# Performance work log

Measured on AMD Instinct MI355X. Metric: run time of the kernel, lower is better.

Reference implementation:

```python
import jax, jax.numpy as jnp
import numpy as np

N = 100000      # nodes
E = 1600000     # edges (before self-loops)
IN_DIM = 128
HID = 32
HEADS = 4
OUT_DIM = 64
NEG_SLOPE = 0.2  # PyG GATConv default


def setup_inputs() -> dict:
    key = jax.random.key(0)
    ks = jax.random.split(key, 12)
    s1 = 1.0 / np.sqrt(IN_DIM).astype(np.float32)
    s2 = 1.0 / np.sqrt(HEADS * HID).astype(np.float32)
    return {
        "x": jax.random.normal(ks[0], (N, IN_DIM), jnp.float32),
        "edge_index": jax.random.randint(ks[1], (2, E), 0, N, dtype=jnp.int64),
        "W1": jax.random.normal(ks[2], (IN_DIM, HEADS * HID), jnp.float32) * s1,
        "att_src1": jax.random.normal(ks[3], (HEADS, HID), jnp.float32) * 0.1,
        "att_dst1": jax.random.normal(ks[4], (HEADS, HID), jnp.float32) * 0.1,
        "b1": jnp.zeros((HEADS * HID,), jnp.float32),
        "W2": jax.random.normal(ks[5], (HEADS * HID, OUT_DIM), jnp.float32) * s2,
        "att_src2": jax.random.normal(ks[6], (1, OUT_DIM), jnp.float32) * 0.1,
        "att_dst2": jax.random.normal(ks[7], (1, OUT_DIM), jnp.float32) * 0.1,
        "b2": jnp.zeros((OUT_DIM,), jnp.float32),
    }


def _gat_layer(x, src, dst, W, att_src, att_dst, bias, heads, out_ch, concat):
    # x: [N, F_in] -> h: [N, H, C]
    n = x.shape[0]
    h = (x @ W).reshape(n, heads, out_ch)
    # per-node attention logits, [N, H]
    a_src = jnp.einsum("nhc,hc->nh", h, att_src)
    a_dst = jnp.einsum("nhc,hc->nh", h, att_dst)
    # edge logits + LeakyReLU, [E, H]
    e = a_src[src] + a_dst[dst]
    e = jnp.where(e >= 0, e, NEG_SLOPE * e)
    # segment softmax over incoming edges of each dst node
    m = jax.ops.segment_max(e, dst, num_segments=n)          # [N, H]
    e = jnp.exp(e - m[dst])
    denom = jax.ops.segment_sum(e, dst, num_segments=n)      # [N, H]
    alpha = e / (denom[dst] + 1e-16)                          # [E, H]
    # weighted scatter-aggregate of source messages -> [N, H, C]
    out = jax.ops.segment_sum(h[src] * alpha[:, :, None], dst, num_segments=n)
    if concat:
        out = out.reshape(n, heads * out_ch)
    else:
        out = out.mean(axis=1)
    return out + bias


def reference(x, edge_index, W1, att_src1, att_dst1, b1, W2, att_src2, att_dst2, b2):
    n = x.shape[0]
    # PyG GATConv adds self-loops by default
    loops = jnp.arange(n, dtype=edge_index.dtype)
    src = jnp.concatenate([edge_index[0], loops])
    dst = jnp.concatenate([edge_index[1], loops])
    h = _gat_layer(x, src, dst, W1, att_src1, att_dst1, b1, HEADS, HID, concat=True)
    h = jax.nn.elu(h)
    # dropout p=0.5 is identity in eval mode (training=False)
    out = _gat_layer(h, src, dst, W2, att_src2, att_dst2, b2, 1, OUT_DIM, concat=False)
    return out
```

## Files before the change

kernel.cpp:

```cpp
#include <hip/hip_runtime.h>
#include <hip/hip_bf16.h>
#include <hip/hip_fp16.h>

#define NEG 0.2f
#define L2E 1.44269504f
#define BSH 9
#define BNODES 512
#define MAXC 16384
#define CHUNK 4096

typedef __attribute__((ext_vector_type(8))) _Float16 half8v;
typedef __attribute__((ext_vector_type(4))) short short4v;
typedef __attribute__((ext_vector_type(4))) float f32x4;

__device__ __forceinline__ float leaky(float e) { return fmaxf(e, NEG * e); }
__device__ __forceinline__ ushort f2h(float f) {
    __half h = __float2half(f);
    return *reinterpret_cast<ushort*>(&h);
}
__device__ __forceinline__ float edgep(float l, float adv, float e0) {
    return __builtin_amdgcn_exp2f(leaky(l + adv) - e0);
}

__device__ __forceinline__ void fma8(float* acc, float a, uint4 h) {
    unsigned wv[4] = { h.x, h.y, h.z, h.w };
    #pragma unroll
    for (int j = 0; j < 4; j++) {
        __half2 hh = *reinterpret_cast<__half2*>(&wv[j]);
        float lo = __half2float(__low2half(hh));
        float hi = __half2float(__high2half(hh));
        acc[2 * j]     = fmaf(a, lo, acc[2 * j]);
        acc[2 * j + 1] = fmaf(a, hi, acc[2 * j + 1]);
    }
}


__global__ void k_zerob(int* __restrict__ bcnt) {
    bcnt[threadIdx.x] = 0;
}

__global__ __launch_bounds__(256) void k_bucket(const int* __restrict__ src, const int* __restrict__ dst,
                                                int E, unsigned int* __restrict__ bbuf,
                                                int* __restrict__ bcnt) {
    __shared__ int hcnt[256], hoff[256], gbase[256], sh[256];
    __shared__ unsigned int lbuf[CHUNK];
    __shared__ unsigned char map[CHUNK];
    int tid = threadIdx.x;
    hcnt[tid] = 0;
    __syncthreads();
    int e0 = blockIdx.x * CHUNK;
    unsigned int pk[16];
    int sl[16];
    unsigned char bb[16];
    #pragma unroll
    for (int r = 0; r < 16; r++) {
        int i = e0 + r * 256 + tid;
        sl[r] = -1; pk[r] = 0; bb[r] = 0;
        if (i < E) {
            int s = src[i], d = dst[i];
            int b = d >> BSH;
            pk[r] = ((unsigned int)(d & (BNODES - 1)) << 17) | (unsigned int)s;
            bb[r] = (unsigned char)b;
            sl[r] = atomicAdd(&hcnt[b], 1);
        }
    }
    __syncthreads();
    int v = hcnt[tid];
    sh[tid] = v;
    __syncthreads();
    for (int off = 1; off < 256; off <<= 1) {
        int t = (tid >= off) ? sh[tid - off] : 0;
        __syncthreads();
        sh[tid] += t;
        __syncthreads();
    }
    hoff[tid] = sh[tid] - v;
    if (v > 0) gbase[tid] = atomicAdd(&bcnt[tid], v);
    __syncthreads();
    #pragma unroll
    for (int r = 0; r < 16; r++) {
        if (sl[r] >= 0) {
            int pos = hoff[bb[r]] + sl[r];
            lbuf[pos] = pk[r];
            map[pos] = bb[r];
        }
    }
    int total = sh[255];
    __syncthreads();
    for (int j = tid; j < total; j += 256) {
        int lo = map[j];
        int p = gbase[lo] + (j - hoff[lo]);
        if (p < MAXC) bbuf[(size_t)lo * MAXC + p] = lbuf[j];
    }
}

__global__ __launch_bounds__(256) void k_hist(const unsigned int* __restrict__ bbuf,
                                              const int* __restrict__ bcnt, int n,
                                              int* __restrict__ deg) {
    __shared__ int hist[BNODES];
    int b = blockIdx.x, tid = threadIdx.x;
    hist[tid] = 0; hist[tid + 256] = 0;
    __syncthreads();
    int cnt = min(bcnt[b], MAXC);
    const unsigned int* p = bbuf + (size_t)b * MAXC;
    for (int i = tid; i < cnt; i += 256) atomicAdd(&hist[p[i] >> 17], 1);
    __syncthreads();
    int n0 = b << BSH;
    if (n0 + tid < n) deg[n0 + tid] = hist[tid];
    if (n0 + 256 + tid < n) deg[n0 + 256 + tid] = hist[tid + 256];
}

__global__ void k_scan1(const int* __restrict__ deg, int n, int* __restrict__ rs, int* __restrict__ bsum) {
    __shared__ int sh[256];
    int tid = threadIdx.x;
    int base = blockIdx.x * 1024 + tid * 4;
    int v0 = (base + 0 < n) ? deg[base + 0] : 0;
    int v1 = (base + 1 < n) ? deg[base + 1] : 0;
    int v2 = (base + 2 < n) ? deg[base + 2] : 0;
    int v3 = (base + 3 < n) ? deg[base + 3] : 0;
    int s = v0 + v1 + v2 + v3;
    sh[tid] = s;
    __syncthreads();
    for (int off = 1; off < 256; off <<= 1) {
        int t = (tid >= off) ? sh[tid - off] : 0;
        __syncthreads();
        sh[tid] += t;
        __syncthreads();
    }
    int ex = sh[tid] - s;
    if (base + 0 < n) rs[base + 0] = ex;
    if (base + 1 < n) rs[base + 1] = ex + v0;
    if (base + 2 < n) rs[base + 2] = ex + v0 + v1;
    if (base + 3 < n) rs[base + 3] = ex + v0 + v1 + v2;
    if (tid == 255) bsum[blockIdx.x] = sh[255];
}

__global__ void k_scan2(int* __restrict__ bsum, int nb) {
    __shared__ int sh[256];
    int tid = threadIdx.x;
    int v = (tid < nb) ? bsum[tid] : 0;
    sh[tid] = v;
    __syncthreads();
    for (int off = 1; off < 256; off <<= 1) {
        int t = (tid >= off) ? sh[tid - off] : 0;
        __syncthreads();
        sh[tid] += t;
        __syncthreads();
    }
    if (tid < nb) bsum[tid] = sh[tid] - v;
}

__global__ void k_scan3(int* __restrict__ rs, const int* __restrict__ bsum, int n, int E) {
    int i = blockIdx.x * blockDim.x + threadIdx.x;
    if (i < n) rs[i] += bsum[i >> 10];
    if (i == n) rs[n] = E;
}

__global__ __launch_bounds__(256) void k_csr(const unsigned int* __restrict__ bbuf,
                                             const int* __restrict__ bcnt, const int* __restrict__ rs,
                                             int n, int* __restrict__ csr) {
    __shared__ int off[BNODES], cur[BNODES];
    __shared__ unsigned int obuf[MAXC];
    int b = blockIdx.x, tid = threadIdx.x;
    int n0 = b << BSH;
    int segbase = rs[n0];
    off[tid]       = rs[min(n0 + tid, n)] - segbase;
    off[tid + 256] = rs[min(n0 + 256 + tid, n)] - segbase;
    cur[tid] = 0; cur[tid + 256] = 0;
    __syncthreads();
    int cnt = min(bcnt[b], MAXC);
    const unsigned int* p = bbuf + (size_t)b * MAXC;
    for (int i = tid; i < cnt; i += 256) {
        unsigned int e = p[i];
        int l = e >> 17;
        int s = atomicAdd(&cur[l], 1);
        obuf[off[l] + s] = e & 0x1FFFFu;
    }
    __syncthreads();
    for (int i = tid; i < cnt; i += 256) csr[segbase + i] = (int)obuf[i];
}

__global__ __launch_bounds__(256) void k_gemm1(const float* __restrict__ x, const float* __restrict__ W,
                                               const float* __restrict__ attS, const float* __restrict__ attD,
                                               ushort* __restrict__ h1b, float* __restrict__ as1,
                                               float* __restrict__ ad1, int n) {
    __shared__ ushort Wt[128 * 136];
    int tid = threadIdx.x;
    #pragma unroll 4
    for (int it = 0; it < 64; it++) {
        int idx = tid + 256 * it;
        int k = idx >> 7, nn = idx & 127;
        Wt[nn * 136 + k] = f2h(W[idx]);
    }
    __syncthreads();
    int lane = tid & 63;
    int wid = tid >> 6;
    int l15 = lane & 15, g = lane >> 4;
    int R0 = blockIdx.x * 128 + wid * 32;
    f32x4 acc[2][8];
    #pragma unroll
    for (int f = 0; f < 2; f++)
        #pragma unroll
        for (int nf = 0; nf < 8; nf++) acc[f][nf] = (f32x4){0.f, 0.f, 0.f, 0.f};
    size_t mclamp[2];
    mclamp[0] = (size_t)((R0 + l15 < n) ? R0 + l15 : n - 1);
    mclamp[1] = (size_t)((R0 + 16 + l15 < n) ? R0 + 16 + l15 : n - 1);
    #pragma unroll
    for (int ks = 0; ks < 4; ks++) {
        half8v xb[2];
        #pragma unroll
        for (int f = 0; f < 2; f++) {
            const float4* xp = (const float4*)(x + mclamp[f] * 128 + ks * 32 + g * 8);
            float4 a0 = xp[0], a1 = xp[1];
            half8v v;
            v[0] = (_Float16)a0.x; v[1] = (_Float16)a0.y; v[2] = (_Float16)a0.z; v[3] = (_Float16)a0.w;
            v[4] = (_Float16)a1.x; v[5] = (_Float16)a1.y; v[6] = (_Float16)a1.z; v[7] = (_Float16)a1.w;
            xb[f] = v;
        }
        #pragma unroll
        for (int nf = 0; nf < 8; nf++) {
            half8v wv = *(const half8v*)(&Wt[(16 * nf + l15) * 136 + ks * 32 + g * 8]);
            acc[0][nf] = __builtin_amdgcn_mfma_f32_16x16x32_f16(wv, xb[0], acc[0][nf], 0, 0, 0);
            acc[1][nf] = __builtin_amdgcn_mfma_f32_16x16x32_f16(wv, xb[1], acc[1][nf], 0, 0, 0);
        }
    }
    #pragma unroll
    for (int f = 0; f < 2; f++) {
        int m = R0 + 16 * f + l15;
        bool ok = m < n;
        float pS[4] = {0.f, 0.f, 0.f, 0.f}, pD[4] = {0.f, 0.f, 0.f, 0.f};
        #pragma unroll
        for (int nf = 0; nf < 8; nf++) {
            int n0 = 16 * nf + 4 * g;
            f32x4 a = acc[f][nf];
            if (ok) {
                short4v s4;
                s4[0] = (short)f2h(a[0]); s4[1] = (short)f2h(a[1]);
                s4[2] = (short)f2h(a[2]); s4[3] = (short)f2h(a[3]);
                *(short4v*)(h1b + (size_t)m * 128 + n0) = s4;
            }
            float4 vS = *(const float4*)(attS + n0);
            float4 vD = *(const float4*)(attD + n0);
            int hd = nf >> 1;
            pS[hd] += a[0] * vS.x + a[1] * vS.y + a[2] * vS.z + a[3] * vS.w;
            pD[hd] += a[0] * vD.x + a[1] * vD.y + a[2] * vD.z + a[3] * vD.w;
        }
        #pragma unroll
        for (int h = 0; h < 4; h++) {
            pS[h] += __shfl_xor(pS[h], 16, 64); pS[h] += __shfl_xor(pS[h], 32, 64);
            pD[h] += __shfl_xor(pD[h], 16, 64); pD[h] += __shfl_xor(pD[h], 32, 64);
        }
        if (ok && g == 0) {
            *(float4*)(as1 + (size_t)m * 4) = make_float4(pS[0] * L2E, pS[1] * L2E, pS[2] * L2E, pS[3] * L2E);
            *(float4*)(ad1 + (size_t)m * 4) = make_float4(pD[0] * L2E, pD[1] * L2E, pD[2] * L2E, pD[3] * L2E);
        }
    }
}

__global__ __launch_bounds__(256) void k_agg1(const int* __restrict__ rs, const int* __restrict__ csr,
                                              const ushort* __restrict__ h1b,
                                              const float* __restrict__ as1, const float* __restrict__ ad1,
                                              const float* __restrict__ b1,
                                              ushort* __restrict__ o1b, int n) {
    int w = (blockIdx.x * 256 + threadIdx.x) >> 6;
    w = __builtin_amdgcn_readfirstlane(w);
    if (w >= n) return;
    int lane = threadIdx.x & 63;
    int g = lane >> 4, q = lane & 15;
    int hd = q >> 2;
    unsigned qoff = 8u * (unsigned)q;
    float adv = ad1[(unsigned)(w * 4 + hd)];
    float e0 = leaky(as1[(unsigned)(w * 4 + hd)] + adv);
    float acc0[8], acc1[8];
    float den0 = 0.f, den1 = 0.f;
    #pragma unroll
    for (int c = 0; c < 8; c++) { acc0[c] = 0.f; acc1[c] = 0.f; }
    if (g == 0) {
        uint4 hv = *(const uint4*)(h1b + (((unsigned)w << 7) + qoff));
        fma8(acc0, 1.0f, hv);
        den0 = 1.0f;
    }
    int beg = rs[w], end = rs[w + 1];
    int i = beg;
    for (; i + 8 <= end; i += 8) {
        int ea = i + g, eb = i + 4 + g;
        int sa = csr[ea], sb = csr[eb];
        float pa = edgep(as1[(unsigned)(sa * 4 + hd)], adv, e0);
        float pb = edgep(as1[(unsigned)(sb * 4 + hd)], adv, e0);
        uint4 ha = *(const uint4*)(h1b + (((unsigned)sa << 7) + qoff));
        uint4 hb = *(const uint4*)(h1b + (((unsigned)sb << 7) + qoff));
        fma8(acc0, pa, ha);
        fma8(acc1, pb, hb);
        den0 += pa; den1 += pb;
    }
    if (i < end) {
        int ea = i + g;
        int ea2 = min(ea, end - 1);
        int sa = csr[ea2];
        float pa = (ea < end) ? edgep(as1[(unsigned)(sa * 4 + hd)], adv, e0) : 0.f;
        uint4 ha = *(const uint4*)(h1b + (((unsigned)sa << 7) + qoff));
        fma8(acc0, pa, ha);
        den0 += pa;
        if (i + 4 < end) {
            int eb = i + 4 + g;
            int eb2 = min(eb, end - 1);
            int sb = csr[eb2];
            float pb = (eb < end) ? edgep(as1[(unsigned)(sb * 4 + hd)], adv, e0) : 0.f;
            uint4 hb = *(const uint4*)(h1b + (((unsigned)sb << 7) + qoff));
            fma8(acc1, pb, hb);
            den1 += pb;
        }
    }
    float den = den0 + den1;
    den += __shfl_xor(den, 16, 64);
    den += __shfl_xor(den, 32, 64);
    #pragma unroll
    for (int c = 0; c < 8; c++) {
        float v = acc0[c] + acc1[c];
        v += __shfl_xor(v, 16, 64);
        v += __shfl_xor(v, 32, 64);
        acc0[c] = v;
    }
    if (g == 0) {
        float inv = 1.0f / den;
        float4 bv0 = *(const float4*)(b1 + 8 * q);
        float4 bv1 = *(const float4*)(b1 + 8 * q + 4);
        float o[8] = { acc0[0] * inv + bv0.x, acc0[1] * inv + bv0.y,
                       acc0[2] * inv + bv0.z, acc0[3] * inv + bv0.w,
                       acc0[4] * inv + bv1.x, acc0[5] * inv + bv1.y,
                       acc0[6] * inv + bv1.z, acc0[7] * inv + bv1.w };
        ushort st[8];
        #pragma unroll
        for (int c = 0; c < 8; c++) {
            float e = (o[c] > 0.f) ? o[c] : (__expf(o[c]) - 1.f);
            st[c] = f2h(e);
        }
        *(uint4*)(o1b + (((unsigned)w << 7) + qoff)) = *(uint4*)st;
    }
}

__global__ __launch_bounds__(256) void k_gemm2(const ushort* __restrict__ o1b, const float* __restrict__ W,
                                               const float* __restrict__ attS, const float* __restrict__ attD,
                                               ushort* __restrict__ h2b, float* __restrict__ as2,
                                               float* __restrict__ ad2, int n) {
    __shared__ ushort Wt[64 * 136];
    int tid = threadIdx.x;
    #pragma unroll 4
    for (int it = 0; it < 32; it++) {
        int idx = tid + 256 * it;
        int k = idx >> 6, nn = idx & 63;
        Wt[nn * 136 + k] = f2h(W[idx]);
    }
    __syncthreads();
    int lane = tid & 63;
    int wid = tid >> 6;
    int l15 = lane & 15, g = lane >> 4;
    int R0 = blockIdx.x * 128 + wid * 32;
    f32x4 acc[2][4];
    #pragma unroll
    for (int f = 0; f < 2; f++)
        #pragma unroll
        for (int nf = 0; nf < 4; nf++) acc[f][nf] = (f32x4){0.f, 0.f, 0.f, 0.f};
    size_t mclamp[2];
    mclamp[0] = (size_t)((R0 + l15 < n) ? R0 + l15 : n - 1);
    mclamp[1] = (size_t)((R0 + 16 + l15 < n) ? R0 + 16 + l15 : n - 1);
    #pragma unroll
    for (int ks = 0; ks < 4; ks++) {
        half8v xb[2];
        xb[0] = *(const half8v*)(o1b + mclamp[0] * 128 + ks * 32 + g * 8);
        xb[1] = *(const half8v*)(o1b + mclamp[1] * 128 + ks * 32 + g * 8);
        #pragma unroll
        for (int nf = 0; nf < 4; nf++) {
            half8v wv = *(const half8v*)(&Wt[(16 * nf + l15) * 136 + ks * 32 + g * 8]);
            acc[0][nf] = __builtin_amdgcn_mfma_f32_16x16x32_f16(wv, xb[0], acc[0][nf], 0, 0, 0);
            acc[1][nf] = __builtin_amdgcn_mfma_f32_16x16x32_f16(wv, xb[1], acc[1][nf], 0, 0, 0);
        }
    }
    #pragma unroll
    for (int f = 0; f < 2; f++) {
        int m = R0 + 16 * f + l15;
        bool ok = m < n;
        float pS = 0.f, pD = 0.f;
        #pragma unroll
        for (int nf = 0; nf < 4; nf++) {
            int n0 = 16 * nf + 4 * g;
            f32x4 a = acc[f][nf];
            if (ok) {
                short4v s4;
                s4[0] = (short)f2h(a[0]); s4[1] = (short)f2h(a[1]);
                s4[2] = (short)f2h(a[2]); s4[3] = (short)f2h(a[3]);
                *(short4v*)(h2b + (size_t)m * 64 + n0) = s4;
            }
            float4 vS = *(const float4*)(attS + n0);
            float4 vD = *(const float4*)(attD + n0);
            pS += a[0] * vS.x + a[1] * vS.y + a[2] * vS.z + a[3] * vS.w;
            pD += a[0] * vD.x + a[1] * vD.y + a[2] * vD.z + a[3] * vD.w;
        }
        pS += __shfl_xor(pS, 16, 64); pS += __shfl_xor(pS, 32, 64);
        pD += __shfl_xor(pD, 16, 64); pD += __shfl_xor(pD, 32, 64);
        if (ok && g == 0) {
            as2[m] = pS * L2E;
            ad2[m] = pD * L2E;
        }
    }
}

__global__ __launch_bounds__(256) void k_agg2(const int* __restrict__ rs, const int* __restrict__ csr,
                                              const ushort* __restrict__ h2b,
                                              const float* __restrict__ as2, const float* __restrict__ ad2,
                                              const float* __restrict__ b2,
                                              float* __restrict__ out, int n) {
    int w = (blockIdx.x * 256 + threadIdx.x) >> 6;
    w = __builtin_amdgcn_readfirstlane(w);
    if (w >= n) return;
    int lane = threadIdx.x & 63;
    int g = lane >> 3, q = lane & 7;
    unsigned qoff = 8u * (unsigned)q;
    float adv = ad2[w];
    float e0 = leaky(as2[w] + adv);
    float acc0[8], acc1[8];
    float den0 = 0.f, den1 = 0.f;
    #pragma unroll
    for (int c = 0; c < 8; c++) { acc0[c] = 0.f; acc1[c] = 0.f; }
    if (g == 0) {
        uint4 hv = *(const uint4*)(h2b + (((unsigned)w << 6) + qoff));
        fma8(acc0, 1.0f, hv);
        den0 = 1.0f;
    }
    int beg = rs[w], end = rs[w + 1];
    int i = beg;
    for (; i + 16 <= end; i += 16) {
        int ea = i + g, eb = i + 8 + g;
        int sa = csr[ea], sb = csr[eb];
        float pa = edgep(as2[(unsigned)sa], adv, e0);
        float pb = edgep(as2[(unsigned)sb], adv, e0);
        uint4 ha = *(const uint4*)(h2b + (((unsigned)sa << 6) + qoff));
        uint4 hb = *(const uint4*)(h2b + (((unsigned)sb << 6) + qoff));
        fma8(acc0, pa, ha);
        fma8(acc1, pb, hb);
        den0 += pa; den1 += pb;
    }
    for (; i < end; i += 8) {
        int e = i + g;
        int e2 = min(e, end - 1);
        int s = csr[e2];
        float p = (e < end) ? edgep(as2[(unsigned)s], adv, e0) : 0.f;
        uint4 hv = *(const uint4*)(h2b + (((unsigned)s << 6) + qoff));
        fma8(acc0, p, hv);
        den0 += p;
    }
    float den = den0 + den1;
    den += __shfl_xor(den, 8, 64);
    den += __shfl_xor(den, 16, 64);
    den += __shfl_xor(den, 32, 64);
    #pragma unroll
    for (int c = 0; c < 8; c++) {
        float v = acc0[c] + acc1[c];
        v += __shfl_xor(v, 8, 64);
        v += __shfl_xor(v, 16, 64);
        v += __shfl_xor(v, 32, 64);
        acc0[c] = v;
    }
    if (g == 0) {
        float inv = 1.0f / den;
        float4 bv0 = *(const float4*)(b2 + 8 * q);
        float4 bv1 = *(const float4*)(b2 + 8 * q + 4);
        float4 o0 = make_float4(acc0[0] * inv + bv0.x, acc0[1] * inv + bv0.y,
                                acc0[2] * inv + bv0.z, acc0[3] * inv + bv0.w);
        float4 o1 = make_float4(acc0[4] * inv + bv1.x, acc0[5] * inv + bv1.y,
                                acc0[6] * inv + bv1.z, acc0[7] * inv + bv1.w);
        *(float4*)(out + (size_t)w * 64 + 8 * q) = o0;
        *(float4*)(out + (size_t)w * 64 + 8 * q + 4) = o1;
    }
}

extern "C" void kernel_launch(void* const* d_in, const int* in_sizes, int n_in,
                              void* d_out, int out_size, void* d_ws, size_t ws_size,
                              hipStream_t stream) {
    const float* x     = (const float*)d_in[0];
    const int*   ei    = (const int*)d_in[1];
    const float* W1    = (const float*)d_in[2];
    const float* attS1 = (const float*)d_in[3];
    const float* attD1 = (const float*)d_in[4];
    const float* b1    = (const float*)d_in[5];
    const float* W2    = (const float*)d_in[6];
    const float* attS2 = (const float*)d_in[7];
    const float* attD2 = (const float*)d_in[8];
    const float* b2    = (const float*)d_in[9];
    float* out = (float*)d_out;

    int n = in_sizes[0] / 128;
    int E = in_sizes[1] / 2;
    const int* srcp = ei;
    const int* dstp = ei + E;
    int nbuck = (n + BNODES - 1) >> BSH;

    char* ws = (char*)d_ws;
    size_t off = 0;
    auto A = [&](size_t bytes) -> void* {
        void* p = ws + off;
        off = (off + bytes + 255) & ~(size_t)255;
        return p;
    };
    int* rs      = (int*)A((size_t)(n + 1) * 4);
    int* deg     = (int*)A((size_t)n * 4);
    int* bcnt    = (int*)A(1024);
    int* bsum    = (int*)A(1024);
    int* csr     = (int*)A((size_t)E * 4);
    float* as1   = (float*)A((size_t)n * 16);
    float* ad1   = (float*)A((size_t)n * 16);
    float* as2   = (float*)A((size_t)n * 4);
    float* ad2   = (float*)A((size_t)n * 4);
    unsigned int* bbuf = (unsigned int*)A((size_t)nbuck * MAXC * 4);
    ushort* h1b  = (ushort*)A((size_t)n * 128 * 2);
    ushort* o1b  = (ushort*)A((size_t)n * 128 * 2);
    ushort* h2b  = h1b;

    int nb = (n + 1023) / 1024;

    hipLaunchKernelGGL(k_zerob, dim3(1), dim3(256), 0, stream, bcnt);
    hipLaunchKernelGGL(k_bucket, dim3((E + CHUNK - 1) / CHUNK), dim3(256), 0, stream, srcp, dstp, E, bbuf, bcnt);
    hipLaunchKernelGGL(k_hist, dim3(nbuck), dim3(256), 0, stream, bbuf, bcnt, n, deg);
    hipLaunchKernelGGL(k_scan1, dim3(nb), dim3(256), 0, stream, deg, n, rs, bsum);
    hipLaunchKernelGGL(k_scan2, dim3(1), dim3(256), 0, stream, bsum, nb);
    hipLaunchKernelGGL(k_scan3, dim3((n + 1 + 255) / 256), dim3(256), 0, stream, rs, bsum, n, E);
    hipLaunchKernelGGL(k_csr, dim3(nbuck), dim3(256), 0, stream, bbuf, bcnt, rs, n, csr);

    hipLaunchKernelGGL(k_gemm1, dim3((n + 127) / 128), dim3(256), 0, stream, x, W1, attS1, attD1, h1b, as1, ad1, n);
    hipLaunchKernelGGL(k_agg1, dim3((n * 64 + 255) / 256), dim3(256), 0, stream, rs, csr, h1b, as1, ad1, b1, o1b, n);
    hipLaunchKernelGGL(k_gemm2, dim3((n + 127) / 128), dim3(256), 0, stream, o1b, W2, attS2, attD2, h2b, as2, ad2, n);
    hipLaunchKernelGGL(k_agg2, dim3((n * 64 + 255) / 256), dim3(256), 0, stream, rs, csr, h2b, as2, ad2, b2, out, n);
}
```

Baseline: 222.2 us.

## Fuse CSR histogram, scan and scatter into per-bucket kernel with bucket-level scan

Replaces the degree histogram, the three-pass global scan and the CSR scatter kernels with a tiny bucket-count scan plus one fused per-bucket kernel. That kernel builds the local histogram, scans it in shared memory, writes row starts and scatters edges. The zeroing kernel becomes a memset. This cuts four kernel launches and the global deg/rs round trips, at the cost of more shared-memory work per block. The rs[n] value is now the sum of clamped bucket counts rather than E.

Result: faster. 216.6 us (-2.5%).

```diff
diff --git a/kernel.cpp b/kernel.cpp
--- a/kernel.cpp
+++ b/kernel.cpp
@@ -34,10 +34,6 @@
     }
 }
 
-
-__global__ void k_zerob(int* __restrict__ bcnt) {
-    bcnt[threadIdx.x] = 0;
-}
 
 __global__ __launch_bounds__(256) void k_bucket(const int* __restrict__ src, const int* __restrict__ dst,
                                                 int E, unsigned int* __restrict__ bbuf,
@@ -94,87 +90,61 @@
     }
 }
 
-__global__ __launch_bounds__(256) void k_hist(const unsigned int* __restrict__ bbuf,
-                                              const int* __restrict__ bcnt, int n,
-                                              int* __restrict__ deg) {
-    __shared__ int hist[BNODES];
+__global__ void k_scanb(const int* __restrict__ bcnt, int nbuck, int* __restrict__ bbase) {
+    __shared__ int sh[256];
+    int tid = threadIdx.x;
+    int v = (tid < nbuck) ? min(bcnt[tid], MAXC) : 0;
+    sh[tid] = v;
+    __syncthreads();
+    for (int off = 1; off < 256; off <<= 1) {
+        int t = (tid >= off) ? sh[tid - off] : 0;
+        __syncthreads();
+        sh[tid] += t;
+        __syncthreads();
+    }
+    if (tid < nbuck) bbase[tid] = sh[tid] - v;
+}
+
+__global__ __launch_bounds__(256) void k_csrX(const unsigned int* __restrict__ bbuf,
+                                              const int* __restrict__ bcnt, const int* __restrict__ bbase,
+                                              int n, int E, int* __restrict__ rs, int* __restrict__ csr) {
+    __shared__ int hist[BNODES], off[BNODES], cur[BNODES], sh[256];
+    __shared__ unsigned int obuf[MAXC];
     int b = blockIdx.x, tid = threadIdx.x;
     hist[tid] = 0; hist[tid + 256] = 0;
+    cur[tid] = 0;  cur[tid + 256] = 0;
     __syncthreads();
     int cnt = min(bcnt[b], MAXC);
     const unsigned int* p = bbuf + (size_t)b * MAXC;
     for (int i = tid; i < cnt; i += 256) atomicAdd(&hist[p[i] >> 17], 1);
     __syncthreads();
+    int h0 = hist[2 * tid], h1v = hist[2 * tid + 1];
+    int s = h0 + h1v;
+    sh[tid] = s;
+    __syncthreads();
+    for (int o = 1; o < 256; o <<= 1) {
+        int t = (tid >= o) ? sh[tid - o] : 0;
+        __syncthreads();
+        sh[tid] += t;
+        __syncthreads();
+    }
+    int ex = sh[tid] - s;
+    off[2 * tid] = ex;
+    off[2 * tid + 1] = ex + h0;
+    __syncthreads();
+    int total = sh[255];
+    int segbase = bbase[b];
     int n0 = b << BSH;
-    if (n0 + tid < n) deg[n0 + tid] = hist[tid];
-    if (n0 + 256 + tid < n) deg[n0 + 256 + tid] = hist[tid + 256];
-}
-
-__global__ void k_scan1(const int* __restrict__ deg, int n, int* __restrict__ rs, int* __restrict__ bsum) {
-    __shared__ int sh[256];
-    int tid = threadIdx.x;
-    int base = blockIdx.x * 1024 + tid * 4;
-    int v0 = (base + 0 < n) ? deg[base + 0] : 0;
-    int v1 = (base + 1 < n) ? deg[base + 1] : 0;
-    int v2 = (base + 2 < n) ? deg[base + 2] : 0;
-    int v3 = (base + 3 < n) ? deg[base + 3] : 0;
-    int s = v0 + v1 + v2 + v3;
-    sh[tid] = s;
-    __syncthreads();
-    for (int off = 1; off < 256; off <<= 1) {
-        int t = (tid >= off) ? sh[tid - off] : 0;
-        __syncthreads();
-        sh[tid] += t;
-        __syncthreads();
-    }
-    int ex = sh[tid] - s;
-    if (base + 0 < n) rs[base + 0] = ex;
-    if (base + 1 < n) rs[base + 1] = ex + v0;
-    if (base + 2 < n) rs[base + 2] = ex + v0 + v1;
-    if (base + 3 < n) rs[base + 3] = ex + v0 + v1 + v2;
-    if (tid == 255) bsum[blockIdx.x] = sh[255];
-}
-
-__global__ void k_scan2(int* __restrict__ bsum, int nb) {
-    __shared__ int sh[256];
-    int tid = threadIdx.x;
-    int v = (tid < nb) ? bsum[tid] : 0;
-    sh[tid] = v;
-    __syncthreads();
-    for (int off = 1; off < 256; off <<= 1) {
-        int t = (tid >= off) ? sh[tid - off] : 0;
-        __syncthreads();
-        sh[tid] += t;
-        __syncthreads();
-    }
-    if (tid < nb) bsum[tid] = sh[tid] - v;
-}
-
-__global__ void k_scan3(int* __restrict__ rs, const int* __restrict__ bsum, int n, int E) {
-    int i = blockIdx.x * blockDim.x + threadIdx.x;
-    if (i < n) rs[i] += bsum[i >> 10];
-    if (i == n) rs[n] = E;
-}
-
-__global__ __launch_bounds__(256) void k_csr(const unsigned int* __restrict__ bbuf,
-                                             const int* __restrict__ bcnt, const int* __restrict__ rs,
-                                             int n, int* __restrict__ csr) {
-    __shared__ int off[BNODES], cur[BNODES];
-    __shared__ unsigned int obuf[MAXC];
-    int b = blockIdx.x, tid = threadIdx.x;
-    int n0 = b << BSH;
-    int segbase = rs[n0];
-    off[tid]       = rs[min(n0 + tid, n)] - segbase;
-    off[tid + 256] = rs[min(n0 + 256 + tid, n)] - segbase;
-    cur[tid] = 0; cur[tid + 256] = 0;
-    __syncthreads();
-    int cnt = min(bcnt[b], MAXC);
-    const unsigned int* p = bbuf + (size_t)b * MAXC;
+    for (int l = tid; l < BNODES; l += 256) {
+        int node = n0 + l;
+        if (node < n) rs[node] = segbase + off[l];
+    }
+    if (b == gridDim.x - 1 && tid == 0) rs[n] = segbase + total;
     for (int i = tid; i < cnt; i += 256) {
         unsigned int e = p[i];
         int l = e >> 17;
-        int s = atomicAdd(&cur[l], 1);
-        obuf[off[l] + s] = e & 0x1FFFFu;
+        int s2 = atomicAdd(&cur[l], 1);
+        obuf[off[l] + s2] = e & 0x1FFFFu;
     }
     __syncthreads();
     for (int i = tid; i < cnt; i += 256) csr[segbase + i] = (int)obuf[i];
@@ -503,9 +473,8 @@
         return p;
     };
     int* rs      = (int*)A((size_t)(n + 1) * 4);
-    int* deg     = (int*)A((size_t)n * 4);
     int* bcnt    = (int*)A(1024);
-    int* bsum    = (int*)A(1024);
+    int* bbase   = (int*)A(1024);
     int* csr     = (int*)A((size_t)E * 4);
     float* as1   = (float*)A((size_t)n * 16);
     float* ad1   = (float*)A((size_t)n * 16);
@@ -516,15 +485,10 @@
     ushort* o1b  = (ushort*)A((size_t)n * 128 * 2);
     ushort* h2b  = h1b;
 
-    int nb = (n + 1023) / 1024;
-
-    hipLaunchKernelGGL(k_zerob, dim3(1), dim3(256), 0, stream, bcnt);
+    hipMemsetAsync(bcnt, 0, 1024, stream);
     hipLaunchKernelGGL(k_bucket, dim3((E + CHUNK - 1) / CHUNK), dim3(256), 0, stream, srcp, dstp, E, bbuf, bcnt);
-    hipLaunchKernelGGL(k_hist, dim3(nbuck), dim3(256), 0, stream, bbuf, bcnt, n, deg);
-    hipLaunchKernelGGL(k_scan1, dim3(nb), dim3(256), 0, stream, deg, n, rs, bsum);
-    hipLaunchKernelGGL(k_scan2, dim3(1), dim3(256), 0, stream, bsum, nb);
-    hipLaunchKernelGGL(k_scan3, dim3((n + 1 + 255) / 256), dim3(256), 0, stream, rs, bsum, n, E);
-    hipLaunchKernelGGL(k_csr, dim3(nbuck), dim3(256), 0, stream, bbuf, bcnt, rs, n, csr);
+    hipLaunchKernelGGL(k_scanb, dim3(1), dim3(256), 0, stream, bcnt, nbuck, bbase);
+    hipLaunchKernelGGL(k_csrX, dim3(nbuck), dim3(256), 0, stream, bbuf, bcnt, bbase, n, E, rs, csr);
 
     hipLaunchKernelGGL(k_gemm1, dim3((n + 127) / 128), dim3(256), 0, stream, x, W1, attS1, attD1, h1b, as1, ad1, n);
     hipLaunchKernelGGL(k_agg1, dim3((n * 64 + 255) / 256), dim3(256), 0, stream, rs, csr, h1b, as1, ad1, b1, o1b, n);
```
